# Kernel tuning notes

Measured on AMD Instinct MI355X. Metric: run time of the kernel, lower is better.

Reference implementation:

```python
import jax, jax.numpy as jnp
import numpy as np

N_NODES = 50000
N_EDGES = 800000
IN_C, HID_C, OUT_C = 256, 256, 128


def gcn_conv(x, W, b, row, col, n_nodes):
    """PyG GCNConv: linear transform, symmetric-normalized aggregation, bias.
    row/col already include self-loops. Messages flow row -> col."""
    h = x @ W  # [N, out]
    deg = jax.ops.segment_sum(jnp.ones_like(col, dtype=h.dtype), col, num_segments=n_nodes)
    d_inv_sqrt = jnp.where(deg > 0, jax.lax.rsqrt(jnp.maximum(deg, 1e-12)), 0.0)
    norm = d_inv_sqrt[row] * d_inv_sqrt[col]  # [E]
    msg = h[row] * norm[:, None]              # gather + scale, [E, out]
    out = jax.ops.segment_sum(msg, col, num_segments=n_nodes)  # scatter-add
    return out + b


def setup_inputs() -> dict:
    key = jax.random.key(0)
    k_x, k_e, k_w1, k_w2 = jax.random.split(key, 4)
    x = jax.random.normal(k_x, (N_NODES, IN_C), dtype=jnp.float32)
    edge_index = jax.random.randint(k_e, (2, N_EDGES), 0, N_NODES, dtype=jnp.int64)
    # Glorot-style init for GCN weights, zeros bias (PyG default)
    s1 = float(np.sqrt(6.0 / (IN_C + HID_C)))
    s2 = float(np.sqrt(6.0 / (HID_C + OUT_C)))
    W1 = jax.random.uniform(k_w1, (IN_C, HID_C), dtype=jnp.float32, minval=-s1, maxval=s1)
    b1 = jnp.zeros((HID_C,), dtype=jnp.float32)
    W2 = jax.random.uniform(k_w2, (HID_C, OUT_C), dtype=jnp.float32, minval=-s2, maxval=s2)
    b2 = jnp.zeros((OUT_C,), dtype=jnp.float32)
    return {"x": x, "edge_index": edge_index, "W1": W1, "b1": b1, "W2": W2, "b2": b2}


def reference(x, edge_index, W1, b1, W2, b2):
    n = x.shape[0]
    # add self-loops (PyG GCNConv default add_self_loops=True)
    loops = jnp.arange(n, dtype=edge_index.dtype)
    row = jnp.concatenate([edge_index[0], loops])
    col = jnp.concatenate([edge_index[1], loops])
    h = gcn_conv(x, W1, b1, row, col, n)
    h = jax.nn.relu(h)  # dropout p=0.0 -> identity
    out = gcn_conv(h, W2, b2, row, col, n)
    return out
```

## Files before the change

kernel.cpp:

```cpp
#include <hip/hip_runtime.h>

#define NN 50000
#define NE 800000
#define IN_C 256
#define HID_C 256
#define OUT_C 128

#define NBUCK 196
#define CHUNK 4096
#define NPA 196
#define CAP_B 5120

typedef unsigned short u16;
typedef __attribute__((ext_vector_type(8))) short short8;
typedef __attribute__((ext_vector_type(8))) unsigned short ushort8;
typedef __attribute__((ext_vector_type(4))) float f32x4;
typedef __attribute__((ext_vector_type(2))) float f32x2;

#define CPS ((size_t)(NN + 1) * 32)

__device__ __forceinline__ u16 f2b(float f) {
  unsigned int u = __float_as_uint(f);
  return (u16)((u + 0x7FFFu + ((u >> 16) & 1u)) >> 16);
}
__device__ __forceinline__ float b2f(u16 s) {
  return __uint_as_float(((unsigned int)s) << 16);
}


__global__ __launch_bounds__(256) void convw_zero(const float* __restrict__ W1,
                                                  const float* __restrict__ W2,
                                                  u16* __restrict__ W1t,
                                                  u16* __restrict__ W2t,
                                                  int* __restrict__ cnt,
                                                  u16* __restrict__ Hb,
                                                  int nzb) {
  int b = blockIdx.x;
  if (b < 256) {
    int id = b * 256 + threadIdx.x;
    if (id < 256 * 256) {
      int n = id >> 8, k = id & 255;
      W1t[id] = f2b(W1[k * 256 + n]);
    }
    if (id < 128 * 256) {
      int n = id >> 8, k = id & 255;
      W2t[id] = f2b(W2[k * 128 + n]);
    }
  } else if (b < 256 + nzb) {
    int i = (b - 256) * 256 + threadIdx.x;
    if (i < NN) cnt[i] = 0;
  } else {
    int t = threadIdx.x;
    Hb[(size_t)(t >> 5) * CPS + (size_t)NN * 32 + (t & 31)] = 0;
  }
}


__global__ __launch_bounds__(256) void hist_kernel(const int* __restrict__ col,
                                                   int* __restrict__ cnt, int E) {
  int e = blockIdx.x * blockDim.x + threadIdx.x;
  if (e < E) atomicAdd(&cnt[col[e]], 1);
}

__global__ __launch_bounds__(256) void scan1_kernel(const int* __restrict__ cnt,
                                                    int* __restrict__ bsum, int n) {
  __shared__ int ws[4];
  int i = blockIdx.x * 256 + threadIdx.x;
  int lane = threadIdx.x & 63, wid = threadIdx.x >> 6;
  int v = (i < n) ? cnt[i] : 0;
#pragma unroll
  for (int off = 32; off > 0; off >>= 1) v += __shfl_down(v, off, 64);
  if (lane == 0) ws[wid] = v;
  __syncthreads();
  if (threadIdx.x == 0) bsum[blockIdx.x] = ws[0] + ws[1] + ws[2] + ws[3];
}

__global__ __launch_bounds__(256) void scan2_kernel(const int* __restrict__ bsum,
                                                    int* __restrict__ boff,
                                                    int* __restrict__ row_off,
                                                    int nb, int n) {
  __shared__ int wsum[4], wpre[5];
  int lane = threadIdx.x & 63, wid = threadIdx.x >> 6;
  int v = (threadIdx.x < nb) ? bsum[threadIdx.x] : 0;
  int s = v;
#pragma unroll
  for (int off = 1; off < 64; off <<= 1) {
    int t = __shfl_up(s, off, 64);
    if (lane >= off) s += t;
  }
  if (lane == 63) wsum[wid] = s;
  __syncthreads();
  if (threadIdx.x == 0) {
    int acc = 0;
#pragma unroll
    for (int w = 0; w < 4; ++w) { wpre[w] = acc; acc += wsum[w]; }
    wpre[4] = acc;
  }
  __syncthreads();
  if (threadIdx.x < nb) boff[threadIdx.x] = wpre[wid] + (s - v);
  if (threadIdx.x == 0) row_off[n] = wpre[4];
}

__global__ __launch_bounds__(256) void scan3_kernel(const int* __restrict__ cnt,
                                                    const int* __restrict__ boff,
                                                    int* __restrict__ row_off,
                                                    int* __restrict__ bcur,
                                                    float* __restrict__ dinv, int n) {
  __shared__ int wsum[4], wpre[4];
  int i = blockIdx.x * 256 + threadIdx.x;
  int lane = threadIdx.x & 63, wid = threadIdx.x >> 6;
  int v = (i < n) ? cnt[i] : 0;
  int s = v;
#pragma unroll
  for (int off = 1; off < 64; off <<= 1) {
    int t = __shfl_up(s, off, 64);
    if (lane >= off) s += t;
  }
  if (lane == 63) wsum[wid] = s;
  __syncthreads();
  if (threadIdx.x == 0) {
    int acc = 0;
#pragma unroll
    for (int w = 0; w < 4; ++w) { wpre[w] = acc; acc += wsum[w]; }
  }
  __syncthreads();
  if (i < n) {
    int off = boff[blockIdx.x] + wpre[wid] + (s - v);
    row_off[i] = off;
    if ((i & 255) == 0) bcur[i >> 8] = off;
    dinv[i] = rsqrtf((float)(v + 1));
  }
}


template <bool A_IS_F32, bool PLANAR_C>
__device__ __forceinline__ void gemm_body(const void* __restrict__ Ap,
                                          const u16* __restrict__ Bt,
                                          const float* __restrict__ dscale,
                                          u16* __restrict__ C, int M, int N,
                                          int bx, int by,
                                          u16 (&Asl)[2][5120], u16 (&Bsl)[2][5120]) {
  const int tid = threadIdx.x;
  const int row0 = by * 128;
  const int col0 = bx * 128;

  f32x4 acc[4][4] = {};

  const int seg = tid & 7;
  const int rb = tid >> 3;
  const int wave = tid >> 6, lane = tid & 63;
  const int wm = wave >> 1, wn = wave & 1;
  const int qr = lane & 15, quad = lane >> 4;

  float4 aF[4];
  ushort4 aU[4];
  ushort4 bR[4];

  auto load_tiles = [&](int k0) {
    if constexpr (A_IS_F32) {
      const float* A = (const float*)Ap;
#pragma unroll
      for (int i = 0; i < 4; ++i) {
        int gr = row0 + rb + i * 32;
        aF[i] = (gr < M) ? *(const float4*)&A[(size_t)gr * 256 + k0 + seg * 4]
                         : make_float4(0.f, 0.f, 0.f, 0.f);
      }
    } else {
      const u16* A = (const u16*)Ap;
#pragma unroll
      for (int i = 0; i < 4; ++i) {
        int gr = row0 + rb + i * 32;
        aU[i] = (gr < M) ? *(const ushort4*)&A[(size_t)gr * 256 + k0 + seg * 4]
                         : make_ushort4(0, 0, 0, 0);
      }
    }
#pragma unroll
    for (int i = 0; i < 4; ++i) {
      int n = rb + i * 32;
      bR[i] = *(const ushort4*)&Bt[(size_t)(col0 + n) * 256 + k0 + seg * 4];
    }
  };

  auto write_lds = [&](int buf) {
#pragma unroll
    for (int i = 0; i < 4; ++i) {
      int r = rb + i * 32;
      ushort4 u;
      if constexpr (A_IS_F32) {
        u.x = f2b(aF[i].x); u.y = f2b(aF[i].y);
        u.z = f2b(aF[i].z); u.w = f2b(aF[i].w);
      } else {
        u = aU[i];
      }
      *(ushort4*)&Asl[buf][r * 40 + seg * 4] = u;
      *(ushort4*)&Bsl[buf][r * 40 + seg * 4] = bR[i];
    }
  };

  load_tiles(0);
  write_lds(0);
  __syncthreads();

#pragma unroll
  for (int it = 0; it < 8; ++it) {
    const int cur = it & 1;
    if (it < 7) load_tiles((it + 1) * 32);

    short8 afr[4], bfr[4];
#pragma unroll
    for (int mt = 0; mt < 4; ++mt)
      afr[mt] = *(const short8*)&Asl[cur][(wm * 64 + mt * 16 + qr) * 40 + quad * 8];
#pragma unroll
    for (int nt = 0; nt < 4; ++nt)
      bfr[nt] = *(const short8*)&Bsl[cur][(wn * 64 + nt * 16 + qr) * 40 + quad * 8];
#pragma unroll
    for (int mt = 0; mt < 4; ++mt)
#pragma unroll
      for (int nt = 0; nt < 4; ++nt)
        acc[mt][nt] = __builtin_amdgcn_mfma_f32_16x16x32_bf16(afr[mt], bfr[nt], acc[mt][nt], 0, 0, 0);

    if (it < 7) {
      write_lds(1 - cur);
      __syncthreads();
    }
  }

#pragma unroll
  for (int mt = 0; mt < 4; ++mt) {
#pragma unroll
    for (int i = 0; i < 4; ++i) {
      int gr = row0 + wm * 64 + mt * 16 + quad * 4 + i;
      if (gr < M) {
        float sc = dscale[gr];
#pragma unroll
        for (int nt = 0; nt < 4; ++nt) {
          int gc = col0 + wn * 64 + nt * 16 + qr;
          u16 val = f2b(acc[mt][nt][i] * sc);
          if constexpr (PLANAR_C)
            C[(size_t)(gc >> 5) * CPS + (size_t)gr * 32 + (gc & 31)] = val;
          else
            C[(size_t)gr * N + gc] = val;
        }
      }
    }
  }
}

template <bool A_IS_F32, bool PLANAR_C>
__global__ __launch_bounds__(256) void gemm_mfma(const void* __restrict__ Ap,
                                                 const u16* __restrict__ Bt,
                                                 const float* __restrict__ dscale,
                                                 u16* __restrict__ C, int M, int N,
                                                 u16* __restrict__ zrow) {
  if (zrow != nullptr && blockIdx.x == 0 && blockIdx.y == 0 && threadIdx.x < 128) {
    int t = threadIdx.x;
    zrow[(size_t)(t >> 5) * CPS + (size_t)NN * 32 + (t & 31)] = 0;
  }
  __shared__ u16 Asl[2][5120];
  __shared__ u16 Bsl[2][5120];
  gemm_body<A_IS_F32, PLANAR_C>(Ap, Bt, dscale, C, M, N, blockIdx.x, blockIdx.y, Asl, Bsl);
}

__global__ __launch_bounds__(256) void gemm1_scatter(const float* __restrict__ x,
                                                     const u16* __restrict__ W1t,
                                                     const float* __restrict__ dinv,
                                                     u16* __restrict__ Hb, int M, int N,
                                                     int ngb,
                                                     const int* __restrict__ row,
                                                     const int* __restrict__ col,
                                                     int* __restrict__ bcur,
                                                     uint2* __restrict__ stage, int E) {
  __shared__ u16 ABsl[4][5120];
  int b = blockIdx.x;
  if (b < ngb) {
    gemm_body<true, true>(x, W1t, dinv, Hb, M, N, b & 1, b >> 1,
                          *reinterpret_cast<u16(*)[2][5120]>(&ABsl[0]),
                          *reinterpret_cast<u16(*)[2][5120]>(&ABsl[2]));
  } else {
    uint2* pairs = (uint2*)ABsl;
    int* hcnt = (int*)((char*)ABsl + 32768);
    int* hscan = hcnt + 256;
    int* hbase = hscan + 256;
    int* lcur = hbase + 256;

    const int tid = threadIdx.x;
    const int blk = b - ngb;
    const int e0 = blk * CHUNK;

    hcnt[tid] = 0;
    __syncthreads();

    int ecol[16], erow[16];
#pragma unroll
    for (int j = 0; j < 16; ++j) {
      int e = e0 + j * 256 + tid;
      if (e < E) {
        ecol[j] = col[e];
        erow[j] = row[e];
        atomicAdd(&hcnt[ecol[j] >> 8], 1);
      } else {
        ecol[j] = -1;
      }
    }
    __syncthreads();

    hscan[tid] = hcnt[tid];
    __syncthreads();
#pragma unroll
    for (int off = 1; off < 256; off <<= 1) {
      int t = (tid >= off) ? hscan[tid - off] : 0;
      __syncthreads();
      hscan[tid] += t;
      __syncthreads();
    }

    lcur[tid] = 0;
    if (hcnt[tid] > 0) hbase[tid] = atomicAdd(&bcur[tid], hcnt[tid]);
    __syncthreads();

#pragma unroll
    for (int j = 0; j < 16; ++j) {
      if (ecol[j] >= 0) {
        int bk = ecol[j] >> 8;
        int p = atomicAdd(&lcur[bk], 1);
        pairs[(hscan[bk] - hcnt[bk]) + p] = make_uint2((unsigned)erow[j], (unsigned)ecol[j]);
      }
    }
    __syncthreads();

    int mtot = hscan[255];
    for (int s = tid; s < mtot; s += 256) {
      uint2 pr = pairs[s];
      int bk = (int)(pr.y >> 8);
      stage[hbase[bk] + (s - (hscan[bk] - hcnt[bk]))] = pr;
    }
  }
}

__global__ __launch_bounds__(256) void csr_sort(const uint2* __restrict__ stage,
                                                const int* __restrict__ row_off,
                                                int* __restrict__ csr) {
  __shared__ int cur[256];
  __shared__ int outb[CAP_B];
  const int b = blockIdx.x;
  const int base_node = b << 8;
  const int nnodes = min(256, NN - base_node);
  const int tid = threadIdx.x;
  const int bstart = row_off[base_node];
  const int bend = row_off[min(base_node + 256, NN)];
  if (tid < nnodes) cur[tid] = row_off[base_node + tid] - bstart;
  __syncthreads();
  const int m = bend - bstart;
  for (int i = tid; i < m; i += 256) {
    uint2 pr = stage[bstart + i];
    int cl = min((int)pr.y - base_node, 255) & 255;
    int p = atomicAdd(&cur[cl], 1);
    if (p < CAP_B) outb[p] = (int)pr.x;
    else if (bstart + p < NE) csr[bstart + p] = (int)pr.x;
  }
  __syncthreads();
  const int mm = min(m, CAP_B);
  for (int i = tid; i < mm; i += 256) csr[bstart + i] = outb[i];
}


template <int NPL, int OUTC, bool RELU_BF16>
__global__ __launch_bounds__(256) void agg_planar(const u16* __restrict__ h,
                                                  const int* __restrict__ row_off,
                                                  const int* __restrict__ csr,
                                                  const float* __restrict__ dinv,
                                                  const float* __restrict__ bias,
                                                  void* __restrict__ outp) {
  const int slice = blockIdx.x % NPL;
  const int wave = threadIdx.x >> 6;
  const int lane = threadIdx.x & 63;
  const int nd = lane >> 4;
  const int l4 = lane & 15;
  const int eg = l4 >> 2;
  const int co = l4 & 3;
  const int coff = co * 8;
  const int v = (blockIdx.x / NPL) * 16 + wave * 4 + nd;
  const u16* hpl = h + (size_t)slice * CPS;
  const int beg = row_off[v], end = row_off[v + 1];
  const int sb = (lane & 48) + eg;

  f32x2 accp[4] = {};
  for (int base = beg; base < end; base += 16) {
    int p = base + l4;
    int idx = (p < end) ? csr[p] : NN;
#pragma unroll
    for (int j = 0; j < 4; ++j) {
      unsigned s = (unsigned)__shfl(idx, sb + j * 4, 64);
      ushort8 g = *(const ushort8*)&hpl[(size_t)s * 32 + coff];
      const unsigned* w = (const unsigned*)&g;
#pragma unroll
      for (int q = 0; q < 4; ++q) {
        f32x2 val;
        val[0] = __uint_as_float(w[q] << 16);
        val[1] = __uint_as_float(w[q] & 0xffff0000u);
        accp[q] += val;
      }
    }
  }
  float a[8];
#pragma unroll
  for (int q = 0; q < 4; ++q) { a[2 * q] = accp[q][0]; a[2 * q + 1] = accp[q][1]; }
#pragma unroll
  for (int i = 0; i < 8; ++i) {
    a[i] += __shfl_xor(a[i], 4, 64);
    a[i] += __shfl_xor(a[i], 8, 64);
  }
  if (eg == 0) {
    const int cg = slice * 32 + coff;
    ushort8 hs = *(const ushort8*)&hpl[(size_t)v * 32 + coff];
    float dv = dinv[v];
    float4 bv0 = *(const float4*)&bias[cg];
    float4 bv1 = *(const float4*)&bias[cg + 4];
    float bb[8] = {bv0.x, bv0.y, bv0.z, bv0.w, bv1.x, bv1.y, bv1.z, bv1.w};
    if constexpr (RELU_BF16) {
      u16* out = (u16*)outp;
      ushort8 o;
#pragma unroll
      for (int i = 0; i < 8; ++i) {
        float r = fmaxf((a[i] + b2f((u16)hs[i])) * dv + bb[i], 0.f);
        o[i] = (short)f2b(r);
      }
      *(ushort8*)&out[(size_t)v * OUTC + cg] = o;
    } else {
      float* out = (float*)outp;
      float o[8];
#pragma unroll
      for (int i = 0; i < 8; ++i) o[i] = (a[i] + b2f((u16)hs[i])) * dv + bb[i];
      *(float4*)&out[(size_t)v * OUTC + cg] = make_float4(o[0], o[1], o[2], o[3]);
      *(float4*)&out[(size_t)v * OUTC + cg + 4] = make_float4(o[4], o[5], o[6], o[7]);
    }
  }
}


extern "C" void kernel_launch(void* const* d_in, const int* in_sizes, int n_in,
                              void* d_out, int out_size, void* d_ws, size_t ws_size,
                              hipStream_t stream) {
  const float* x = (const float*)d_in[0];
  const int* ei = (const int*)d_in[1];
  const float* W1 = (const float*)d_in[2];
  const float* b1 = (const float*)d_in[3];
  const float* W2 = (const float*)d_in[4];
  const float* b2 = (const float*)d_in[5];
  float* out = (float*)d_out;

  const int* row = ei;
  const int* col = ei + NE;

  const int NB = (NN + 255) / 256;

  u16* Hb = (u16*)d_ws;
  u16* H2b = Hb + (size_t)(NN + 1) * 256;
  u16* H3b = H2b + (size_t)NN * 256;
  u16* W1t = H3b + (size_t)(NN + 1) * 128;
  u16* W2t = W1t + 256 * 256;
  int* cnt = (int*)(W2t + 128 * 256);
  int* row_off = cnt + NN;
  int* bcur = row_off + NN + 4;
  float* dinv = (float*)(bcur + 256);
  int* bsum = (int*)(dinv + NN);
  int* boff = bsum + 200;
  int* csr = boff + 200;
  uint2* stage = (uint2*)H3b;

  convw_zero<<<256 + NB + 1, 256, 0, stream>>>(W1, W2, W1t, W2t, cnt, Hb, NB);
  hist_kernel<<<(NE + 255) / 256, 256, 0, stream>>>(col, cnt, NE);
  scan1_kernel<<<NB, 256, 0, stream>>>(cnt, bsum, NN);
  scan2_kernel<<<1, 256, 0, stream>>>(bsum, boff, row_off, NB, NN);
  scan3_kernel<<<NB, 256, 0, stream>>>(cnt, boff, row_off, bcur, dinv, NN);

  {
    const int ngb = (HID_C / 128) * ((NN + 127) / 128);
    gemm1_scatter<<<ngb + NPA, 256, 0, stream>>>(x, W1t, dinv, Hb, NN, HID_C, ngb,
                                                 row, col, bcur, stage, NE);
  }
  csr_sort<<<NBUCK, 256, 0, stream>>>(stage, row_off, csr);

  agg_planar<8, 256, true><<<(NN / 16) * 8, 256, 0, stream>>>(
      Hb, row_off, csr, dinv, b1, H2b);

  {
    dim3 grid(OUT_C / 128, (NN + 127) / 128);
    gemm_mfma<false, true><<<grid, 256, 0, stream>>>(H2b, W2t, dinv, H3b, NN, OUT_C, H3b);
  }

  agg_planar<4, 128, false><<<(NN / 16) * 4, 256, 0, stream>>>(
      H3b, row_off, csr, dinv, b2, out);
}
```

Baseline: 272.8 us.

## Aggregate neighbor features with MFMA one-hot matrices over 16-node groups

Replaces the per-node shuffle-and-add aggregation with a per-wave scheme over 16-node groups. Gathered neighbor rows are transposed through LDS with ds_read_b64_tr_b16, and an MFMA is run with a one-hot selection matrix built from destination tags packed into the CSR entries. Self-loops now go into the CSR as explicit edges (counts start at 1) instead of being added separately. This aims to cut scalar accumulation and shuffle-reduction work and to process 32 edges per step. In exchange it relies on 16-bit packed source indices (valid because NN < 65536), inline assembly, and unaligned vector loads of the CSR.

```diff
diff --git a/kernel.cpp b/kernel.cpp
--- a/kernel.cpp
+++ b/kernel.cpp
@@ -6,16 +6,21 @@
 #define HID_C 256
 #define OUT_C 128
 
+#define NET (NE + NN)
 #define NBUCK 196
 #define CHUNK 4096
 #define NPA 196
 #define CAP_B 5120
+#define NGRP (NN / 16)
 
 typedef unsigned short u16;
+typedef unsigned int u32;
 typedef __attribute__((ext_vector_type(8))) short short8;
+typedef __attribute__((ext_vector_type(4))) short short4_t;
 typedef __attribute__((ext_vector_type(8))) unsigned short ushort8;
 typedef __attribute__((ext_vector_type(4))) float f32x4;
-typedef __attribute__((ext_vector_type(2))) float f32x2;
+typedef __attribute__((ext_vector_type(4))) unsigned u32x4;
+typedef __attribute__((ext_vector_type(4), aligned(4))) unsigned u32x4u;
 
 #define CPS ((size_t)(NN + 1) * 32)
 
@@ -48,7 +53,7 @@
     }
   } else if (b < 256 + nzb) {
     int i = (b - 256) * 256 + threadIdx.x;
-    if (i < NN) cnt[i] = 0;
+    if (i < NN) cnt[i] = 1;
   } else {
     int t = threadIdx.x;
     Hb[(size_t)(t >> 5) * CPS + (size_t)NN * 32 + (t & 31)] = 0;
@@ -128,7 +133,7 @@
     int off = boff[blockIdx.x] + wpre[wid] + (s - v);
     row_off[i] = off;
     if ((i & 255) == 0) bcur[i >> 8] = off;
-    dinv[i] = rsqrtf((float)(v + 1));
+    dinv[i] = rsqrtf((float)v);
   }
 }
 
@@ -339,100 +344,108 @@
 
 __global__ __launch_bounds__(256) void csr_sort(const uint2* __restrict__ stage,
                                                 const int* __restrict__ row_off,
-                                                int* __restrict__ csr) {
+                                                u32* __restrict__ csrp) {
   __shared__ int cur[256];
-  __shared__ int outb[CAP_B];
+  __shared__ u32 outb[CAP_B];
   const int b = blockIdx.x;
   const int base_node = b << 8;
   const int nnodes = min(256, NN - base_node);
   const int tid = threadIdx.x;
   const int bstart = row_off[base_node];
   const int bend = row_off[min(base_node + 256, NN)];
-  if (tid < nnodes) cur[tid] = row_off[base_node + tid] - bstart;
+  if (tid < nnodes) {
+    int c0 = row_off[base_node + tid] - bstart;
+    outb[c0] = (u32)(base_node + tid) | ((u32)(tid & 15) << 16);
+    cur[tid] = c0 + 1;
+  }
   __syncthreads();
   const int m = bend - bstart;
-  for (int i = tid; i < m; i += 256) {
+  const int mreal = m - nnodes;
+  for (int i = tid; i < mreal; i += 256) {
     uint2 pr = stage[bstart + i];
-    int cl = min((int)pr.y - base_node, 255) & 255;
+    int cl = ((int)pr.y - base_node) & 255;
     int p = atomicAdd(&cur[cl], 1);
-    if (p < CAP_B) outb[p] = (int)pr.x;
-    else if (bstart + p < NE) csr[bstart + p] = (int)pr.x;
+    u32 val = (pr.x & 0xFFFFu) | ((u32)(cl & 15) << 16);
+    if (p < CAP_B) outb[p] = val;
+    else if (bstart + p < NET) csrp[bstart + p] = val;
   }
   __syncthreads();
   const int mm = min(m, CAP_B);
-  for (int i = tid; i < mm; i += 256) csr[bstart + i] = outb[i];
-}
-
+  for (int i = tid; i < mm; i += 256) csrp[bstart + i] = outb[i];
+}
 
 template <int NPL, int OUTC, bool RELU_BF16>
-__global__ __launch_bounds__(256) void agg_planar(const u16* __restrict__ h,
-                                                  const int* __restrict__ row_off,
-                                                  const int* __restrict__ csr,
-                                                  const float* __restrict__ dinv,
-                                                  const float* __restrict__ bias,
-                                                  void* __restrict__ outp) {
+__global__ __launch_bounds__(256) void agg_mfma(const u16* __restrict__ h,
+                                                const int* __restrict__ row_off,
+                                                const u32* __restrict__ csrp,
+                                                const float* __restrict__ dinv,
+                                                const float* __restrict__ bias,
+                                                void* __restrict__ outp) {
+  __shared__ char lds[4][2048];
   const int slice = blockIdx.x % NPL;
   const int wave = threadIdx.x >> 6;
+  const int g = (blockIdx.x / NPL) * 4 + wave;
+  if (g >= NGRP) return;
   const int lane = threadIdx.x & 63;
-  const int nd = lane >> 4;
-  const int l4 = lane & 15;
-  const int eg = l4 >> 2;
-  const int co = l4 & 3;
-  const int coff = co * 8;
-  const int v = (blockIdx.x / NPL) * 16 + wave * 4 + nd;
+  const int qr = lane & 15, quad = lane >> 4;
+  const int s = lane >> 1, half = lane & 1;
   const u16* hpl = h + (size_t)slice * CPS;
-  const int beg = row_off[v], end = row_off[v + 1];
-  const int sb = (lane & 48) + eg;
-
-  f32x2 accp[4] = {};
-  for (int base = beg; base < end; base += 16) {
-    int p = base + l4;
-    int idx = (p < end) ? csr[p] : NN;
+  const int beg = row_off[g * 16];
+  const int end = row_off[g * 16 + 16];
+  char* wl = lds[wave];
+  char* wp = wl + (half * 1024 + ((s >> 2) & 1) * 512 + (s >> 3) * 128 + (s & 3) * 32);
+  const unsigned trb = (unsigned)(size_t)(wl) + (unsigned)(lane * 8);
+
+  f32x4 acc0 = {}, acc1 = {};
+  for (int base = beg; base < end; base += 32) {
+    int p = base + s;
+    unsigned src = (p < end) ? (csrp[p] & 0xFFFFu) : (unsigned)NN;
+    const u16* rp = hpl + (size_t)src * 32 + half * 16;
+    u32x4 d0 = *(const u32x4*)rp;
+    u32x4 d1 = *(const u32x4*)(rp + 8);
+    u32x4u w0 = *(const u32x4u*)&csrp[base + quad * 8];
+    u32x4u w1 = *(const u32x4u*)&csrp[base + quad * 8 + 4];
+    short8 afr;
 #pragma unroll
     for (int j = 0; j < 4; ++j) {
-      unsigned s = (unsigned)__shfl(idx, sb + j * 4, 64);
-      ushort8 g = *(const ushort8*)&hpl[(size_t)s * 32 + coff];
-      const unsigned* w = (const unsigned*)&g;
-#pragma unroll
-      for (int q = 0; q < 4; ++q) {
-        f32x2 val;
-        val[0] = __uint_as_float(w[q] << 16);
-        val[1] = __uint_as_float(w[q] & 0xffff0000u);
-        accp[q] += val;
-      }
-    }
-  }
-  float a[8];
-#pragma unroll
-  for (int q = 0; q < 4; ++q) { a[2 * q] = accp[q][0]; a[2 * q + 1] = accp[q][1]; }
-#pragma unroll
-  for (int i = 0; i < 8; ++i) {
-    a[i] += __shfl_xor(a[i], 4, 64);
-    a[i] += __shfl_xor(a[i], 8, 64);
-  }
-  if (eg == 0) {
-    const int cg = slice * 32 + coff;
-    ushort8 hs = *(const ushort8*)&hpl[(size_t)v * 32 + coff];
-    float dv = dinv[v];
-    float4 bv0 = *(const float4*)&bias[cg];
-    float4 bv1 = *(const float4*)&bias[cg + 4];
-    float bb[8] = {bv0.x, bv0.y, bv0.z, bv0.w, bv1.x, bv1.y, bv1.z, bv1.w};
+      afr[j]     = (short)(((w0[j] >> 16) == (unsigned)qr) ? 0x3F80 : 0);
+      afr[j + 4] = (short)(((w1[j] >> 16) == (unsigned)qr) ? 0x3F80 : 0);
+    }
+    *(u32x4*)wp = d0;
+    *(u32x4*)(wp + 16) = d1;
+    short4_t t00, t01, t10, t11;
+    asm volatile("s_waitcnt lgkmcnt(0)\n\t"
+                 "ds_read_b64_tr_b16 %0, %4 offset:0\n\t"
+                 "ds_read_b64_tr_b16 %1, %4 offset:512\n\t"
+                 "ds_read_b64_tr_b16 %2, %4 offset:1024\n\t"
+                 "ds_read_b64_tr_b16 %3, %4 offset:1536\n\t"
+                 "s_waitcnt lgkmcnt(0)"
+                 : "=&v"(t00), "=&v"(t01), "=&v"(t10), "=&v"(t11)
+                 : "v"(trb)
+                 : "memory");
+    __builtin_amdgcn_sched_barrier(0);
+    short8 b0 = __builtin_shufflevector(t00, t01, 0, 1, 2, 3, 4, 5, 6, 7);
+    short8 b1 = __builtin_shufflevector(t10, t11, 0, 1, 2, 3, 4, 5, 6, 7);
+    acc0 = __builtin_amdgcn_mfma_f32_16x16x32_bf16(afr, b0, acc0, 0, 0, 0);
+    acc1 = __builtin_amdgcn_mfma_f32_16x16x32_bf16(afr, b1, acc1, 0, 0, 0);
+  }
+  const int node0 = g * 16 + quad * 4;
+  const int chb = slice * 32;
+  float bv0 = bias[chb + qr];
+  float bv1 = bias[chb + 16 + qr];
+#pragma unroll
+  for (int i = 0; i < 4; ++i) {
+    float dv = dinv[node0 + i];
+    float r0 = acc0[i] * dv + bv0;
+    float r1 = acc1[i] * dv + bv1;
     if constexpr (RELU_BF16) {
-      u16* out = (u16*)outp;
-      ushort8 o;
-#pragma unroll
-      for (int i = 0; i < 8; ++i) {
-        float r = fmaxf((a[i] + b2f((u16)hs[i])) * dv + bb[i], 0.f);
-        o[i] = (short)f2b(r);
-      }
-      *(ushort8*)&out[(size_t)v * OUTC + cg] = o;
+      u16* o = (u16*)outp;
+      o[(size_t)(node0 + i) * OUTC + chb + qr] = f2b(fmaxf(r0, 0.f));
+      o[(size_t)(node0 + i) * OUTC + chb + 16 + qr] = f2b(fmaxf(r1, 0.f));
     } else {
-      float* out = (float*)outp;
-      float o[8];
-#pragma unroll
-      for (int i = 0; i < 8; ++i) o[i] = (a[i] + b2f((u16)hs[i])) * dv + bb[i];
-      *(float4*)&out[(size_t)v * OUTC + cg] = make_float4(o[0], o[1], o[2], o[3]);
-      *(float4*)&out[(size_t)v * OUTC + cg + 4] = make_float4(o[4], o[5], o[6], o[7]);
+      float* o = (float*)outp;
+      o[(size_t)(node0 + i) * OUTC + chb + qr] = r0;
+      o[(size_t)(node0 + i) * OUTC + chb + 16 + qr] = r1;
     }
   }
 }
@@ -465,7 +478,7 @@
   float* dinv = (float*)(bcur + 256);
   int* bsum = (int*)(dinv + NN);
   int* boff = bsum + 200;
-  int* csr = boff + 200;
+  u32* csrp = (u32*)(boff + 200);
   uint2* stage = (uint2*)H3b;
 
   convw_zero<<<256 + NB + 1, 256, 0, stream>>>(W1, W2, W1t, W2t, cnt, Hb, NB);
@@ -479,16 +492,17 @@
     gemm1_scatter<<<ngb + NPA, 256, 0, stream>>>(x, W1t, dinv, Hb, NN, HID_C, ngb,
                                                  row, col, bcur, stage, NE);
   }
-  csr_sort<<<NBUCK, 256, 0, stream>>>(stage, row_off, csr);
-
-  agg_planar<8, 256, true><<<(NN / 16) * 8, 256, 0, stream>>>(
-      Hb, row_off, csr, dinv, b1, H2b);
+  csr_sort<<<NBUCK, 256, 0, stream>>>(stage, row_off, csrp);
+
+  const int NG4 = (NGRP + 3) / 4;
+  agg_mfma<8, 256, true><<<NG4 * 8, 256, 0, stream>>>(
+      Hb, row_off, csrp, dinv, b1, H2b);
 
   {
     dim3 grid(OUT_C / 128, (NN + 127) / 128);
     gemm_mfma<false, true><<<grid, 256, 0, stream>>>(H2b, W2t, dinv, H3b, NN, OUT_C, H3b);
   }
 
-  agg_planar<4, 128, false><<<(NN / 16) * 4, 256, 0, stream>>>(
-      H3b, row_off, csr, dinv, b2, out);
-}
+  agg_mfma<4, 128, false><<<NG4 * 4, 256, 0, stream>>>(
+      H3b, row_off, csrp, dinv, b2, out);
+}
```

After: 277.9 us. No clear change (+1.9%).
